# Kernel optimization log

Measured on AMD Instinct MI355X. Metric: run time of the kernel, lower is better.

Reference implementation:

```python
import jax, jax.numpy as jnp
import numpy as np

N, E, NFEAT, NHID, H = 25000, 400000, 256, 32, 12
NEG_SLOPE = 0.2


def setup_inputs() -> dict:
    key = jax.random.key(0)
    ks = jax.random.split(key, 16)
    g = lambda k, shp, s=0.05: jax.random.normal(k, shp, dtype=jnp.float32) * s
    return {
        "x": jax.random.normal(ks[0], (N, NFEAT), dtype=jnp.float32),
        "edge_index": jax.random.randint(ks[1], (2, E), 0, N, dtype=jnp.int64),
        "edge_attr": jax.random.normal(ks[2], (E, NHID), dtype=jnp.float32),
        # conv1: in=NFEAT -> H heads x NHID, edge_dim=NHID, concat=True
        "W1": g(ks[3], (NFEAT, H * NHID)),
        "att_src1": g(ks[4], (H, NHID)),
        "att_dst1": g(ks[5], (H, NHID)),
        "W_e1": g(ks[6], (NHID, H * NHID)),
        "att_edge1": g(ks[7], (H, NHID)),
        "b1": jnp.zeros((H * NHID,), jnp.float32),
        # conv2: in=H*NHID -> H heads x NHID, concat=False (mean over heads)
        "W2": g(ks[8], (H * NHID, H * NHID)),
        "att_src2": g(ks[9], (H, NHID)),
        "att_dst2": g(ks[10], (H, NHID)),
        "b2": jnp.zeros((NHID,), jnp.float32),
    }


def gat_layer(x, edge_index, W, att_src, att_dst, bias, concat,
              edge_attr=None, W_e=None, att_e=None):
    n = x.shape[0]
    h, c = att_src.shape
    hx = (x @ W).reshape(n, h, c)                      # [N,H,C]
    a_s = jnp.sum(hx * att_src, axis=-1)               # [N,H]
    a_d = jnp.sum(hx * att_dst, axis=-1)               # [N,H]
    src, dst = edge_index[0], edge_index[1]
    loop = jnp.arange(n)
    if edge_attr is not None:
        # PyG add_self_loops fill_value='mean': mean of incoming edge_attr per dst
        cnt = jax.ops.segment_sum(jnp.ones(dst.shape[0], jnp.float32), dst, n)
        loop_attr = jax.ops.segment_sum(edge_attr, dst, n) / jnp.maximum(cnt, 1.0)[:, None]
        edge_attr = jnp.concatenate([edge_attr, loop_attr], axis=0)
    src = jnp.concatenate([src, loop])
    dst = jnp.concatenate([dst, loop])
    e = a_s[src] + a_d[dst]                            # [E+N,H]
    if edge_attr is not None:
        he = (edge_attr @ W_e).reshape(-1, h, c)
        e = e + jnp.sum(he * att_e, axis=-1)
    e = jax.nn.leaky_relu(e, NEG_SLOPE)
    # segment softmax over destination nodes (every node has a self loop -> no empty segments)
    m = jax.ops.segment_max(e, dst, n)                 # [N,H]
    ex = jnp.exp(e - m[dst])
    den = jax.ops.segment_sum(ex, dst, n)
    alpha = ex / den[dst]                              # [E+N,H]
    out = jax.ops.segment_sum(alpha[:, :, None] * hx[src], dst, n)  # [N,H,C]
    out = out.reshape(n, h * c) if concat else out.mean(axis=1)
    return out + bias


def reference(x, edge_index, edge_attr, W1, att_src1, att_dst1, W_e1, att_edge1, b1,
              W2, att_src2, att_dst2, b2):
    # eval mode: all F.dropout / GATConv dropout are identity
    h1 = gat_layer(x, edge_index, W1, att_src1, att_dst1, b1, True,
                   edge_attr, W_e1, att_edge1)
    h1 = jax.nn.elu(h1)
    h2 = gat_layer(h1, edge_index, W2, att_src2, att_dst2, b2, False)
    return h2, jax.nn.log_softmax(h2, axis=1)
```

## Files before the change

kernel.cpp:

```cpp
#include <hip/hip_runtime.h>
#include <hip/hip_bf16.h>
#include <math.h>

#define N_NODES 25000
#define N_EDGES 400000
#define NFEAT   256
#define NHID    32
#define NHEAD   12
#define HC      384
#define HCX     416
#define NEG_SLOPE 0.2f
#define NBLK    ((N_NODES + 255) / 256)
#define BPAD    40

typedef __attribute__((ext_vector_type(8))) short short8;
typedef __attribute__((ext_vector_type(4))) float floatx4;

__device__ __forceinline__ float bf2f(unsigned short u) {
    union { unsigned int i; float f; } v; v.i = ((unsigned int)u) << 16; return v.f;
}
__device__ __forceinline__ unsigned short f2bf(float f) {
    union { float f; unsigned int i; } v; v.f = f;
    unsigned int x = v.i;
    unsigned int r = (x + 0x7FFFu + ((x >> 16) & 1u)) >> 16;
    return (unsigned short)r;
}
__device__ __forceinline__ int clampN(int s) {
    return ((unsigned)s < (unsigned)N_NODES) ? s : 0;
}
__device__ __forceinline__ float ldf(const void* p, size_t i, int isF32) {
    return isF32 ? ((const float*)p)[i] : bf2f(((const unsigned short*)p)[i]);
}
__device__ __forceinline__ int ldi(const void* p, size_t i, int isI64) {
    return isI64 ? (int)((const unsigned int*)p)[2 * i] : ((const int*)p)[i];
}

__device__ __forceinline__ void fma8(float* acc, float a, uint4 g) {
    unsigned int u[4] = {g.x, g.y, g.z, g.w};
#pragma unroll
    for (int i = 0; i < 4; i++) {
        union { unsigned int i; float f; } lo, hi;
        lo.i = u[i] << 16;
        hi.i = u[i] & 0xFFFF0000u;
        acc[2 * i]     += a * lo.f;
        acc[2 * i + 1] += a * hi.f;
    }
}
__device__ __forceinline__ void mul8(float* acc, float a, uint4 g) {
    unsigned int u[4] = {g.x, g.y, g.z, g.w};
#pragma unroll
    for (int i = 0; i < 4; i++) {
        union { unsigned int i; float f; } lo, hi;
        lo.i = u[i] << 16;
        hi.i = u[i] & 0xFFFF0000u;
        acc[2 * i]     = a * lo.f;
        acc[2 * i + 1] = a * hi.f;
    }
}

__global__ void detect_kernel(const unsigned short* __restrict__ xr,
                              const unsigned int* __restrict__ eir,
                              int* __restrict__ flags) {
    __shared__ int sF, sI;
    if (threadIdx.x == 0) { sF = 0; sI = 0; }
    __syncthreads();
    int t = threadIdx.x;
    int cf = 0, ci = 0;
#pragma unroll
    for (int i = 0; i < 4; i++) {
        unsigned short u = xr[2 * (t * 4 + i)];
        int e = (u >> 7) & 0xFF;
        if (e >= 100 && e <= 140) cf++;
        unsigned int v = eir[2 * (t * 4 + i) + 1];
        if (v == 0u) ci++;
    }
    atomicAdd(&sF, cf);
    atomicAdd(&sI, ci);
    __syncthreads();
    if (threadIdx.x == 0) {
        flags[0] = (sF >= 614) ? 0 : 1;
        flags[1] = (sI >= 512) ? 1 : 0;
    }
}

__global__ void prep_kernel(const void* __restrict__ We1,
                            const void* __restrict__ att_e,
                            const void* __restrict__ W1,
                            const void* __restrict__ W2,
                            const void* __restrict__ as1,
                            const void* __restrict__ ad1,
                            const void* __restrict__ as2,
                            const void* __restrict__ ad2,
                            const int* __restrict__ flags,
                            float* __restrict__ M1,
                            unsigned short* __restrict__ Wt1,
                            unsigned short* __restrict__ Wt2) {
    int isF32 = flags[0];
    int id = blockIdx.x * 256 + threadIdx.x;
    if (id < 384) {
        int k = id / 12, h = id % 12;
        float s = 0.f;
        for (int c = 0; c < 32; c++)
            s += ldf(We1, (size_t)k * HC + h * 32 + c, isF32) *
                 ldf(att_e, (size_t)h * 32 + c, isF32);
        M1[k * 12 + h] = s;
        return;
    }
    int id1 = id - 384;
    if (id1 < HCX * 256) {
        int n = id1 / 256, k = id1 % 256;
        unsigned short v = 0;
        if (n < 384) {
            v = f2bf(ldf(W1, (size_t)k * HC + n, isF32));
        } else if (n < 400) {
            int h = n - 384;
            if (h < 12) {
                float s = 0.f;
                for (int c = 0; c < 32; c++)
                    s += ldf(W1, (size_t)k * HC + h * 32 + c, isF32) *
                         ldf(as1, (size_t)h * 32 + c, isF32);
                v = f2bf(s);
            }
        } else {
            int h = n - 400;
            if (h < 12) {
                float s = 0.f;
                for (int c = 0; c < 32; c++)
                    s += ldf(W1, (size_t)k * HC + h * 32 + c, isF32) *
                         ldf(ad1, (size_t)h * 32 + c, isF32);
                v = f2bf(s);
            }
        }
        Wt1[(size_t)n * 256 + k] = v;
        return;
    }
    int id2 = id1 - HCX * 256;
    if (id2 < HCX * 384) {
        int n = id2 / 384, k = id2 % 384;
        unsigned short v = 0;
        if (n < 384) {
            v = f2bf(ldf(W2, (size_t)k * HC + n, isF32));
        } else if (n < 400) {
            int h = n - 384;
            if (h < 12) {
                float s = 0.f;
                for (int c = 0; c < 32; c++)
                    s += ldf(W2, (size_t)k * HC + h * 32 + c, isF32) *
                         ldf(as2, (size_t)h * 32 + c, isF32);
                v = f2bf(s);
            }
        } else {
            int h = n - 400;
            if (h < 12) {
                float s = 0.f;
                for (int c = 0; c < 32; c++)
                    s += ldf(W2, (size_t)k * HC + h * 32 + c, isF32) *
                         ldf(ad2, (size_t)h * 32 + c, isF32);
                v = f2bf(s);
            }
        }
        Wt2[(size_t)n * 384 + k] = v;
    }
}

__global__ void hist_kernel(const void* __restrict__ ei, const int* __restrict__ flags,
                            int* __restrict__ cnt) {
    int isI64 = flags[1];
    int e = blockIdx.x * 256 + threadIdx.x;
    if (e < N_EDGES) {
        int d = clampN(ldi(ei, (size_t)N_EDGES + e, isI64));
        atomicAdd(&cnt[d], 1);
    }
}

__global__ void blockscan_kernel(const int* __restrict__ cnt, int* __restrict__ incl,
                                 int* __restrict__ bsum) {
    __shared__ int buf[256];
    int i = blockIdx.x * 256 + threadIdx.x;
    int v = (i < N_NODES) ? cnt[i] : 0;
    buf[threadIdx.x] = v;
    __syncthreads();
    for (int off = 1; off < 256; off <<= 1) {
        int t = (threadIdx.x >= off) ? buf[threadIdx.x - off] : 0;
        __syncthreads();
        buf[threadIdx.x] += t;
        __syncthreads();
    }
    if (i < N_NODES) incl[i] = buf[threadIdx.x];
    if (threadIdx.x == 255) bsum[blockIdx.x] = buf[255];
}

__global__ void bscan_kernel(const int* __restrict__ bsum, int* __restrict__ boff) {
    __shared__ int buf[128];
    int t = threadIdx.x;
    int v = (t < NBLK) ? bsum[t] : 0;
    buf[t] = v;
    __syncthreads();
    for (int off = 1; off < 128; off <<= 1) {
        int u = (t >= off) ? buf[t - off] : 0;
        __syncthreads();
        buf[t] += u;
        __syncthreads();
    }
    if (t < NBLK) boff[t] = buf[t] - v;
}

__global__ void finalize_kernel(const int* __restrict__ incl, const int* __restrict__ boff,
                                const int* __restrict__ cnt,
                                int* __restrict__ rowptr, int* __restrict__ wofs) {
    int i = blockIdx.x * 256 + threadIdx.x;
    if (i == 0) rowptr[0] = 0;
    if (i < N_NODES) {
        int v = incl[i] + boff[blockIdx.x];
        rowptr[i + 1] = v;
        wofs[i] = v - cnt[i];
    }
}

__global__ void scatter_kernel(const void* __restrict__ ei, const int* __restrict__ flags,
                               int* __restrict__ wofs, int2* __restrict__ pairs) {
    int isI64 = flags[1];
    int e = blockIdx.x * 256 + threadIdx.x;
    if (e >= N_EDGES) return;
    int d = clampN(ldi(ei, (size_t)N_EDGES + e, isI64));
    int pos = atomicAdd(&wofs[d], 1);
    if ((unsigned)pos >= (unsigned)N_EDGES) return;
    pairs[pos] = make_int2(clampN(ldi(ei, (size_t)e, isI64)), e);
}

__global__ void ae_kernel(const void* __restrict__ ea, const int* __restrict__ flags,
                          const float* __restrict__ M1,
                          const int2* __restrict__ pairs,
                          unsigned short* __restrict__ ae_edge) {
    __shared__ float sM[384];
    for (int i = threadIdx.x; i < 384; i += 256) sM[i] = M1[i];
    __syncthreads();
    int isF32 = flags[0];
    int p = blockIdx.x * 256 + threadIdx.x;
    if (p >= N_EDGES) return;
    int eid = pairs[p].y;
    if ((unsigned)eid >= (unsigned)N_EDGES) eid = 0;
    float a[32];
    if (isF32) {
        const float4* r4 = (const float4*)((const float*)ea + (size_t)eid * 32);
#pragma unroll
        for (int i = 0; i < 8; i++) {
            float4 v = r4[i];
            a[4 * i] = v.x; a[4 * i + 1] = v.y; a[4 * i + 2] = v.z; a[4 * i + 3] = v.w;
        }
    } else {
        const unsigned short* r = (const unsigned short*)ea + (size_t)eid * 32;
#pragma unroll
        for (int i = 0; i < 32; i++) a[i] = bf2f(r[i]);
    }
    float ev[12];
#pragma unroll
    for (int h = 0; h < 12; h++) ev[h] = 0.f;
#pragma unroll
    for (int k = 0; k < 32; k++)
#pragma unroll
        for (int h = 0; h < 12; h++) ev[h] += a[k] * sM[k * 12 + h];
    unsigned int w[6];
#pragma unroll
    for (int i = 0; i < 6; i++)
        w[i] = (unsigned int)f2bf(ev[2 * i]) | ((unsigned int)f2bf(ev[2 * i + 1]) << 16);
    uint2* dst = (uint2*)(ae_edge + (size_t)p * 12);
    dst[0] = make_uint2(w[0], w[1]);
    dst[1] = make_uint2(w[2], w[3]);
    dst[2] = make_uint2(w[4], w[5]);
}

__global__ __launch_bounds__(512) void gemm_mfma(const void* __restrict__ A,
                                                 const unsigned short* __restrict__ Bt,
                                                 const int* __restrict__ flags,
                                                 int aFromFlag,
                                                 unsigned short* __restrict__ C,
                                                 float* __restrict__ a_s,
                                                 float* __restrict__ a_d,
                                                 int M, int K) {
    __shared__ unsigned short sB[HCX * BPAD];
    int aF32 = aFromFlag ? flags[0] : 0;
    int lane = threadIdx.x & 63;
    int w = threadIdx.x >> 6;
    int m0 = blockIdx.x * 64 + (w >> 1) * 16;
    int c0 = (w & 1) * 192;
    int ecol = 384 + (w & 1) * 16;
    int r = lane & 15, q = lane >> 4;
    int row = m0 + r;
    if (row >= M) row = M - 1;
    floatx4 acc[13];
#pragma unroll
    for (int j = 0; j < 13; j++) acc[j] = (floatx4){0.f, 0.f, 0.f, 0.f};
    for (int k0 = 0; k0 < K; k0 += 32) {
        for (int i = threadIdx.x; i < HCX * 4; i += 512) {
            int col = i >> 2, seg = i & 3;
            *(uint4*)(sB + (size_t)col * BPAD + seg * 8) =
                *(const uint4*)(Bt + (size_t)col * K + k0 + seg * 8);
        }
        __syncthreads();
        short8 a;
        if (aF32) {
            const float4* ap = (const float4*)((const float*)A + (size_t)row * K + k0 + q * 8);
            float4 u = ap[0], v = ap[1];
            a[0] = (short)f2bf(u.x); a[1] = (short)f2bf(u.y);
            a[2] = (short)f2bf(u.z); a[3] = (short)f2bf(u.w);
            a[4] = (short)f2bf(v.x); a[5] = (short)f2bf(v.y);
            a[6] = (short)f2bf(v.z); a[7] = (short)f2bf(v.w);
        } else {
            a = *(const short8*)((const unsigned short*)A + (size_t)row * K + k0 + q * 8);
        }
#pragma unroll
        for (int j = 0; j < 12; j++) {
            int col = c0 + 16 * j + r;
            short8 b = *(const short8*)(sB + (size_t)col * BPAD + q * 8);
            acc[j] = __builtin_amdgcn_mfma_f32_16x16x32_bf16(a, b, acc[j], 0, 0, 0);
        }
        {
            short8 b = *(const short8*)(sB + (size_t)(ecol + r) * BPAD + q * 8);
            acc[12] = __builtin_amdgcn_mfma_f32_16x16x32_bf16(a, b, acc[12], 0, 0, 0);
        }
        __syncthreads();
    }
#pragma unroll
    for (int j = 0; j < 12; j++) {
        int col = c0 + 16 * j + r;
#pragma unroll
        for (int t = 0; t < 4; t++) {
            int orow = m0 + q * 4 + t;
            if (orow < M) C[(size_t)orow * HC + col] = f2bf(acc[j][t]);
        }
    }
    if (r < 12) {
        float* dst = (w & 1) ? a_d : a_s;
#pragma unroll
        for (int t = 0; t < 4; t++) {
            int orow = m0 + q * 4 + t;
            if (orow < M) dst[orow * 12 + r] = acc[12][t];
        }
    }
}

__global__ __launch_bounds__(256) void softmax_kernel(const float* __restrict__ a_s,
                                                      const float* __restrict__ a_d,
                                                      const int* __restrict__ rowptr,
                                                      const int2* __restrict__ pairs,
                                                      const unsigned short* __restrict__ ae_edge,
                                                      unsigned short* __restrict__ alpha_e,
                                                      float* __restrict__ exl_out,
                                                      float* __restrict__ rden_out,
                                                      int has_ae) {
    int id = blockIdx.x * 256 + threadIdx.x;
    if (id >= N_NODES * NHEAD) return;
    int node = id / NHEAD;
    int h = id - node * NHEAD;
    int start = rowptr[node], end = rowptr[node + 1];
    if (start < 0) start = 0;
    if (end > N_EDGES) end = N_EDGES;
    int deg = end - start;
    float adn = a_d[id];
    float asn = a_s[id];
    float mx = -1e30f, sae = 0.f;
    for (int p = start; p < end; p += 2) {
        int2 pe0 = pairs[p];
        bool two = (p + 1 < end);
        int2 pe1 = two ? pairs[p + 1] : pe0;
        int s0 = clampN(pe0.x), s1 = clampN(pe1.x);
        float v0 = a_s[(size_t)s0 * NHEAD + h] + adn;
        float v1 = a_s[(size_t)s1 * NHEAD + h] + adn;
        if (has_ae) {
            float a0 = bf2f(ae_edge[(size_t)p * NHEAD + h]);
            float a1 = two ? bf2f(ae_edge[(size_t)(p + 1) * NHEAD + h]) : 0.f;
            v0 += a0; sae += a0;
            if (two) { v1 += a1; sae += a1; }
        }
        v0 = v0 > 0.f ? v0 : NEG_SLOPE * v0;
        v1 = v1 > 0.f ? v1 : NEG_SLOPE * v1;
        mx = fmaxf(mx, v0);
        if (two) mx = fmaxf(mx, v1);
    }
    float invdeg = 1.f / fmaxf((float)deg, 1.f);
    float el = asn + adn + (has_ae ? sae * invdeg : 0.f);
    el = el > 0.f ? el : NEG_SLOPE * el;
    mx = fmaxf(mx, el);
    float den = 0.f;
    for (int p = start; p < end; p += 2) {
        int2 pe0 = pairs[p];
        bool two = (p + 1 < end);
        int2 pe1 = two ? pairs[p + 1] : pe0;
        int s0 = clampN(pe0.x), s1 = clampN(pe1.x);
        float v0 = a_s[(size_t)s0 * NHEAD + h] + adn;
        float v1 = a_s[(size_t)s1 * NHEAD + h] + adn;
        if (has_ae) {
            v0 += bf2f(ae_edge[(size_t)p * NHEAD + h]);
            if (two) v1 += bf2f(ae_edge[(size_t)(p + 1) * NHEAD + h]);
        }
        v0 = v0 > 0.f ? v0 : NEG_SLOPE * v0;
        v1 = v1 > 0.f ? v1 : NEG_SLOPE * v1;
        float ex0 = expf(v0 - mx);
        float ex1 = expf(v1 - mx);
        alpha_e[(size_t)p * NHEAD + h] = f2bf(ex0);
        den += ex0;
        if (two) {
            alpha_e[(size_t)(p + 1) * NHEAD + h] = f2bf(ex1);
            den += ex1;
        }
    }
    float exl = expf(el - mx);
    exl_out[id] = exl;
    rden_out[id] = 1.f / (den + exl);
}

__global__ __launch_bounds__(256) void agg1_kernel(const unsigned short* __restrict__ hx,
                                                   const unsigned short* __restrict__ alpha_e,
                                                   const float* __restrict__ exl,
                                                   const float* __restrict__ rden,
                                                   const int* __restrict__ rowptr,
                                                   const int2* __restrict__ pairs,
                                                   const void* __restrict__ b1,
                                                   const int* __restrict__ flags,
                                                   unsigned short* __restrict__ h1) {
    int isF32 = flags[0];
    int lane = threadIdx.x & 63;
    int node = blockIdx.x * 4 + (threadIdx.x >> 6);
    if (node >= N_NODES || lane >= 48) return;
    int h = lane >> 2;
    int off = lane * 8;
    int start = rowptr[node], end = rowptr[node + 1];
    if (start < 0) start = 0;
    if (end > N_EDGES) end = N_EDGES;
    float acc[8];
    {
        uint4 g = *(const uint4*)(hx + (size_t)node * HC + off);
        mul8(acc, exl[node * 12 + h], g);
    }
    int p = start;
    int2 pe0, pe1, pe2, pe3;
    bool have = (p + 4 <= end);
    if (have) {
        pe0 = pairs[p]; pe1 = pairs[p + 1]; pe2 = pairs[p + 2]; pe3 = pairs[p + 3];
    }
    while (have) {
        int2 c0 = pe0, c1 = pe1, c2 = pe2, c3 = pe3;
        bool nxt = (p + 8 <= end);
        if (nxt) {
            pe0 = pairs[p + 4]; pe1 = pairs[p + 5]; pe2 = pairs[p + 6]; pe3 = pairs[p + 7];
        }
        uint4 g0 = *(const uint4*)(hx + (size_t)clampN(c0.x) * HC + off);
        uint4 g1 = *(const uint4*)(hx + (size_t)clampN(c1.x) * HC + off);
        uint4 g2 = *(const uint4*)(hx + (size_t)clampN(c2.x) * HC + off);
        uint4 g3 = *(const uint4*)(hx + (size_t)clampN(c3.x) * HC + off);
        float a0 = bf2f(alpha_e[(size_t)p * 12 + h]);
        float a1 = bf2f(alpha_e[(size_t)(p + 1) * 12 + h]);
        float a2 = bf2f(alpha_e[(size_t)(p + 2) * 12 + h]);
        float a3 = bf2f(alpha_e[(size_t)(p + 3) * 12 + h]);
        fma8(acc, a0, g0);
        fma8(acc, a1, g1);
        fma8(acc, a2, g2);
        fma8(acc, a3, g3);
        p += 4;
        have = nxt;
    }
    for (; p < end; p++) {
        int2 pe = pairs[p];
        uint4 g = *(const uint4*)(hx + (size_t)clampN(pe.x) * HC + off);
        float a = bf2f(alpha_e[(size_t)p * 12 + h]);
        fma8(acc, a, g);
    }
    float rd = rden[node * 12 + h];
    unsigned int w[4];
#pragma unroll
    for (int i = 0; i < 4; i++) {
        float v0 = acc[2 * i] * rd + ldf(b1, (size_t)(off + 2 * i), isF32);
        float v1 = acc[2 * i + 1] * rd + ldf(b1, (size_t)(off + 2 * i + 1), isF32);
        v0 = v0 > 0.f ? v0 : expm1f(v0);
        v1 = v1 > 0.f ? v1 : expm1f(v1);
        w[i] = (unsigned int)f2bf(v0) | ((unsigned int)f2bf(v1) << 16);
    }
    *(uint4*)(h1 + (size_t)node * HC + off) = make_uint4(w[0], w[1], w[2], w[3]);
}

__global__ __launch_bounds__(256) void agg2_kernel(const unsigned short* __restrict__ hx,
                                                   const unsigned short* __restrict__ alpha_e,
                                                   const float* __restrict__ exl,
                                                   const float* __restrict__ rden,
                                                   const int* __restrict__ rowptr,
                                                   const int2* __restrict__ pairs,
                                                   const void* __restrict__ b2,
                                                   const int* __restrict__ flags,
                                                   float* __restrict__ out) {
    int isF32 = flags[0];
    int lane = threadIdx.x & 63;
    int node = blockIdx.x * 4 + (threadIdx.x >> 6);
    if (node >= N_NODES) return;
    bool act = lane < 48;
    int h = act ? (lane >> 2) : 0;
    int off = act ? lane * 8 : 0;
    float acc[8];
#pragma unroll
    for (int k = 0; k < 8; k++) acc[k] = 0.f;
    if (act) {
        int start = rowptr[node], end = rowptr[node + 1];
        if (start < 0) start = 0;
        if (end > N_EDGES) end = N_EDGES;
        {
            uint4 g = *(const uint4*)(hx + (size_t)node * HC + off);
            mul8(acc, exl[node * 12 + h], g);
        }
        int p = start;
        int2 pe0, pe1, pe2, pe3;
        bool have = (p + 4 <= end);
        if (have) {
            pe0 = pairs[p]; pe1 = pairs[p + 1]; pe2 = pairs[p + 2]; pe3 = pairs[p + 3];
        }
        while (have) {
            int2 c0 = pe0, c1 = pe1, c2 = pe2, c3 = pe3;
            bool nxt = (p + 8 <= end);
            if (nxt) {
                pe0 = pairs[p + 4]; pe1 = pairs[p + 5]; pe2 = pairs[p + 6]; pe3 = pairs[p + 7];
            }
            uint4 g0 = *(const uint4*)(hx + (size_t)clampN(c0.x) * HC + off);
            uint4 g1 = *(const uint4*)(hx + (size_t)clampN(c1.x) * HC + off);
            uint4 g2 = *(const uint4*)(hx + (size_t)clampN(c2.x) * HC + off);
            uint4 g3 = *(const uint4*)(hx + (size_t)clampN(c3.x) * HC + off);
            float a0 = bf2f(alpha_e[(size_t)p * 12 + h]);
            float a1 = bf2f(alpha_e[(size_t)(p + 1) * 12 + h]);
            float a2 = bf2f(alpha_e[(size_t)(p + 2) * 12 + h]);
            float a3 = bf2f(alpha_e[(size_t)(p + 3) * 12 + h]);
            fma8(acc, a0, g0);
            fma8(acc, a1, g1);
            fma8(acc, a2, g2);
            fma8(acc, a3, g3);
            p += 4;
            have = nxt;
        }
        for (; p < end; p++) {
            int2 pe = pairs[p];
            uint4 g = *(const uint4*)(hx + (size_t)clampN(pe.x) * HC + off);
            float a = bf2f(alpha_e[(size_t)p * 12 + h]);
            fma8(acc, a, g);
        }
        float rd = rden[node * 12 + h];
#pragma unroll
        for (int k = 0; k < 8; k++) acc[k] *= rd;
    }
#pragma unroll
    for (int k = 0; k < 8; k++) {
        float t1 = __shfl(acc[k], lane + 16);
        float t2 = __shfl(acc[k], lane + 32);
        acc[k] += t1 + t2;
        acc[k] += __shfl_xor(acc[k], 4);
        acc[k] += __shfl_xor(acc[k], 8);
    }
    if (lane < 4) {
        int q = lane;
        float hv[8];
        float m = -1e30f;
#pragma unroll
        for (int t = 0; t < 8; t++) {
            hv[t] = acc[t] * (1.f / 12.f) + ldf(b2, (size_t)(8 * q + t), isF32);
            m = fmaxf(m, hv[t]);
        }
        m = fmaxf(m, __shfl_xor(m, 1));
        m = fmaxf(m, __shfl_xor(m, 2));
        float s = 0.f;
#pragma unroll
        for (int t = 0; t < 8; t++) s += expf(hv[t] - m);
        s += __shfl_xor(s, 1);
        s += __shfl_xor(s, 2);
        float ls = m + logf(s);
        float4* o0 = (float4*)(out + (size_t)node * 32 + 8 * q);
        float4* l0 = (float4*)(out + (size_t)N_NODES * 32 + (size_t)node * 32 + 8 * q);
        o0[0] = make_float4(hv[0], hv[1], hv[2], hv[3]);
        o0[1] = make_float4(hv[4], hv[5], hv[6], hv[7]);
        l0[0] = make_float4(hv[0] - ls, hv[1] - ls, hv[2] - ls, hv[3] - ls);
        l0[1] = make_float4(hv[4] - ls, hv[5] - ls, hv[6] - ls, hv[7] - ls);
    }
}

extern "C" void kernel_launch(void* const* d_in, const int* in_sizes, int n_in,
                              void* d_out, int out_size, void* d_ws, size_t ws_size,
                              hipStream_t stream) {
    const void* x        = d_in[0];
    const void* ei       = d_in[1];
    const void* ea       = d_in[2];
    const void* W1       = d_in[3];
    const void* att_src1 = d_in[4];
    const void* att_dst1 = d_in[5];
    const void* We1      = d_in[6];
    const void* att_e1   = d_in[7];
    const void* b1       = d_in[8];
    const void* W2       = d_in[9];
    const void* att_src2 = d_in[10];
    const void* att_dst2 = d_in[11];
    const void* b2       = d_in[12];
    float* out = (float*)d_out;

    char* ws = (char*)d_ws;
    size_t off = 0;
    auto alloc = [&](size_t bytes) -> void* {
        void* p = ws + off;
        off = (off + bytes + 255) & ~(size_t)255;
        return p;
    };
    int*            flags   = (int*)alloc(16);
    float*          M1      = (float*)alloc((size_t)384 * 4);
    int*            rowptr  = (int*)alloc((size_t)(N_NODES + 1) * 4);
    int*            cnt     = (int*)alloc((size_t)N_NODES * 4);
    int*            wofs    = (int*)alloc((size_t)N_NODES * 4);
    int*            incl    = (int*)alloc((size_t)N_NODES * 4);
    int*            bsum    = (int*)alloc((size_t)NBLK * 4);
    int*            boff    = (int*)alloc((size_t)NBLK * 4);
    float*          a_s     = (float*)alloc((size_t)N_NODES * 12 * 4);
    float*          a_d     = (float*)alloc((size_t)N_NODES * 12 * 4);
    float*          exl     = (float*)alloc((size_t)N_NODES * 12 * 4);
    float*          rden    = (float*)alloc((size_t)N_NODES * 12 * 4);
    int2*           pairs   = (int2*)alloc((size_t)N_EDGES * 8);
    unsigned short* alpha_e = (unsigned short*)alloc((size_t)N_EDGES * 12 * 2);
    unsigned short* hx      = (unsigned short*)alloc((size_t)N_NODES * HC * 2);
    unsigned short* h1      = (unsigned short*)alloc((size_t)N_NODES * HC * 2);
    unsigned short* ae_edge = h1;
    unsigned short* Wt1     = (unsigned short*)alloc((size_t)HCX * 256 * 2);
    unsigned short* Wt2     = (unsigned short*)alloc((size_t)HCX * 384 * 2);

    hipMemsetAsync(cnt, 0, (size_t)N_NODES * 4, stream);
    detect_kernel<<<1, 256, 0, stream>>>((const unsigned short*)x, (const unsigned int*)ei, flags);
    prep_kernel<<<(384 + HCX * 256 + HCX * 384 + 255) / 256, 256, 0, stream>>>(
        We1, att_e1, W1, W2, att_src1, att_dst1, att_src2, att_dst2, flags, M1, Wt1, Wt2);
    hist_kernel<<<(N_EDGES + 255) / 256, 256, 0, stream>>>(ei, flags, cnt);
    blockscan_kernel<<<NBLK, 256, 0, stream>>>(cnt, incl, bsum);
    bscan_kernel<<<1, 128, 0, stream>>>(bsum, boff);
    finalize_kernel<<<NBLK, 256, 0, stream>>>(incl, boff, cnt, rowptr, wofs);
    scatter_kernel<<<(N_EDGES + 255) / 256, 256, 0, stream>>>(ei, flags, wofs, pairs);
    ae_kernel<<<(N_EDGES + 255) / 256, 256, 0, stream>>>(ea, flags, M1, pairs, ae_edge);
    gemm_mfma<<<(N_NODES + 63) / 64, 512, 0, stream>>>(x, Wt1, flags, 1, hx, a_s, a_d,
                                                       N_NODES, NFEAT);
    softmax_kernel<<<(N_NODES * 12 + 255) / 256, 256, 0, stream>>>(a_s, a_d, rowptr, pairs,
                                                                   ae_edge, alpha_e, exl, rden, 1);
    agg1_kernel<<<(N_NODES + 3) / 4, 256, 0, stream>>>(hx, alpha_e, exl, rden, rowptr, pairs,
                                                       b1, flags, h1);
    gemm_mfma<<<(N_NODES + 63) / 64, 512, 0, stream>>>(h1, Wt2, flags, 0, hx, a_s, a_d,
                                                       N_NODES, HC);
    softmax_kernel<<<(N_NODES * 12 + 255) / 256, 256, 0, stream>>>(a_s, a_d, rowptr, pairs,
                                                                   ae_edge, alpha_e, exl, rden, 0);
    agg2_kernel<<<(N_NODES + 3) / 4, 256, 0, stream>>>(hx, alpha_e, exl, rden, rowptr, pairs,
                                                       b2, flags, out);
}
```

Baseline: 409.2 us.

## Fuse CSR-building preprocessing kernels to cut launch count

```diff
diff --git a/kernel.cpp b/kernel.cpp
--- a/kernel.cpp
+++ b/kernel.cpp
@@ -10,8 +10,11 @@
 #define HC      384
 #define HCX     416
 #define NEG_SLOPE 0.2f
-#define NBLK    ((N_NODES + 255) / 256)
 #define BPAD    40
+#define PREP_BLKS ((384 + HCX * 256 + HCX * 384 + 255) / 256)
+#define HIST_BLKS ((N_EDGES + 255) / 256)
+#define SCAN_T  1024
+#define SCAN_C  25
 
 typedef __attribute__((ext_vector_type(8))) short short8;
 typedef __attribute__((ext_vector_type(4))) float floatx4;
@@ -60,18 +63,22 @@
 
 __global__ void detect_kernel(const unsigned short* __restrict__ xr,
                               const unsigned int* __restrict__ eir,
-                              int* __restrict__ flags) {
+                              int* __restrict__ flags,
+                              int* __restrict__ cnt) {
+    int i = blockIdx.x * 256 + threadIdx.x;
+    if (i < N_NODES) cnt[i] = 0;
+    if (blockIdx.x != 0) return;
     __shared__ int sF, sI;
     if (threadIdx.x == 0) { sF = 0; sI = 0; }
     __syncthreads();
     int t = threadIdx.x;
     int cf = 0, ci = 0;
 #pragma unroll
-    for (int i = 0; i < 4; i++) {
-        unsigned short u = xr[2 * (t * 4 + i)];
+    for (int k = 0; k < 4; k++) {
+        unsigned short u = xr[2 * (t * 4 + k)];
         int e = (u >> 7) & 0xFF;
         if (e >= 100 && e <= 140) cf++;
-        unsigned int v = eir[2 * (t * 4 + i) + 1];
+        unsigned int v = eir[2 * (t * 4 + k) + 1];
         if (v == 0u) ci++;
     }
     atomicAdd(&sF, cf);
@@ -83,20 +90,32 @@
     }
 }
 
-__global__ void prep_kernel(const void* __restrict__ We1,
-                            const void* __restrict__ att_e,
-                            const void* __restrict__ W1,
-                            const void* __restrict__ W2,
-                            const void* __restrict__ as1,
-                            const void* __restrict__ ad1,
-                            const void* __restrict__ as2,
-                            const void* __restrict__ ad2,
-                            const int* __restrict__ flags,
-                            float* __restrict__ M1,
-                            unsigned short* __restrict__ Wt1,
-                            unsigned short* __restrict__ Wt2) {
+__global__ void prep_hist_kernel(const void* __restrict__ We1,
+                                 const void* __restrict__ att_e,
+                                 const void* __restrict__ W1,
+                                 const void* __restrict__ W2,
+                                 const void* __restrict__ as1,
+                                 const void* __restrict__ ad1,
+                                 const void* __restrict__ as2,
+                                 const void* __restrict__ ad2,
+                                 const void* __restrict__ ei,
+                                 const int* __restrict__ flags,
+                                 float* __restrict__ M1,
+                                 unsigned short* __restrict__ Wt1,
+                                 unsigned short* __restrict__ Wt2,
+                                 int* __restrict__ cnt) {
     int isF32 = flags[0];
-    int id = blockIdx.x * 256 + threadIdx.x;
+    int bid = blockIdx.x;
+    if (bid >= PREP_BLKS) {
+        int isI64 = flags[1];
+        int e = (bid - PREP_BLKS) * 256 + threadIdx.x;
+        if (e < N_EDGES) {
+            int d = clampN(ldi(ei, (size_t)N_EDGES + e, isI64));
+            atomicAdd(&cnt[d], 1);
+        }
+        return;
+    }
+    int id = bid * 256 + threadIdx.x;
     if (id < 384) {
         int k = id / 12, h = id % 12;
         float s = 0.f;
@@ -163,62 +182,53 @@
     }
 }
 
-__global__ void hist_kernel(const void* __restrict__ ei, const int* __restrict__ flags,
-                            int* __restrict__ cnt) {
-    int isI64 = flags[1];
-    int e = blockIdx.x * 256 + threadIdx.x;
-    if (e < N_EDGES) {
-        int d = clampN(ldi(ei, (size_t)N_EDGES + e, isI64));
-        atomicAdd(&cnt[d], 1);
-    }
-}
-
-__global__ void blockscan_kernel(const int* __restrict__ cnt, int* __restrict__ incl,
-                                 int* __restrict__ bsum) {
-    __shared__ int buf[256];
-    int i = blockIdx.x * 256 + threadIdx.x;
-    int v = (i < N_NODES) ? cnt[i] : 0;
-    buf[threadIdx.x] = v;
+__global__ __launch_bounds__(SCAN_T) void scan_kernel(const int* __restrict__ cnt,
+                                                      int* __restrict__ rowptr,
+                                                      int* __restrict__ wofs) {
+    __shared__ int part[SCAN_T];
+    int t = threadIdx.x;
+    int base = t * SCAN_C;
+    int local[SCAN_C];
+    int s = 0;
+#pragma unroll
+    for (int i = 0; i < SCAN_C; i++) {
+        int idx = base + i;
+        int v = (idx < N_NODES) ? cnt[idx] : 0;
+        local[i] = v;
+        s += v;
+    }
+    part[t] = s;
     __syncthreads();
-    for (int off = 1; off < 256; off <<= 1) {
-        int t = (threadIdx.x >= off) ? buf[threadIdx.x - off] : 0;
+    for (int off = 1; off < SCAN_T; off <<= 1) {
+        int u = (t >= off) ? part[t - off] : 0;
         __syncthreads();
-        buf[threadIdx.x] += t;
+        part[t] += u;
         __syncthreads();
     }
-    if (i < N_NODES) incl[i] = buf[threadIdx.x];
-    if (threadIdx.x == 255) bsum[blockIdx.x] = buf[255];
-}
-
-__global__ void bscan_kernel(const int* __restrict__ bsum, int* __restrict__ boff) {
-    __shared__ int buf[128];
-    int t = threadIdx.x;
-    int v = (t < NBLK) ? bsum[t] : 0;
-    buf[t] = v;
+    int run = (t == 0) ? 0 : part[t - 1];
+    if (t == 0) rowptr[0] = 0;
+#pragma unroll
+    for (int i = 0; i < SCAN_C; i++) {
+        int idx = base + i;
+        if (idx < N_NODES) {
+            wofs[idx] = run;
+            run += local[i];
+            rowptr[idx + 1] = run;
+        }
+    }
+}
+
+__global__ void scatter_ae_kernel(const void* __restrict__ ei,
+                                  const void* __restrict__ ea,
+                                  const int* __restrict__ flags,
+                                  const float* __restrict__ M1,
+                                  int* __restrict__ wofs,
+                                  int2* __restrict__ pairs,
+                                  unsigned short* __restrict__ ae_edge) {
+    __shared__ float sM[384];
+    for (int i = threadIdx.x; i < 384; i += 256) sM[i] = M1[i];
     __syncthreads();
-    for (int off = 1; off < 128; off <<= 1) {
-        int u = (t >= off) ? buf[t - off] : 0;
-        __syncthreads();
-        buf[t] += u;
-        __syncthreads();
-    }
-    if (t < NBLK) boff[t] = buf[t] - v;
-}
-
-__global__ void finalize_kernel(const int* __restrict__ incl, const int* __restrict__ boff,
-                                const int* __restrict__ cnt,
-                                int* __restrict__ rowptr, int* __restrict__ wofs) {
-    int i = blockIdx.x * 256 + threadIdx.x;
-    if (i == 0) rowptr[0] = 0;
-    if (i < N_NODES) {
-        int v = incl[i] + boff[blockIdx.x];
-        rowptr[i + 1] = v;
-        wofs[i] = v - cnt[i];
-    }
-}
-
-__global__ void scatter_kernel(const void* __restrict__ ei, const int* __restrict__ flags,
-                               int* __restrict__ wofs, int2* __restrict__ pairs) {
+    int isF32 = flags[0];
     int isI64 = flags[1];
     int e = blockIdx.x * 256 + threadIdx.x;
     if (e >= N_EDGES) return;
@@ -226,30 +236,16 @@
     int pos = atomicAdd(&wofs[d], 1);
     if ((unsigned)pos >= (unsigned)N_EDGES) return;
     pairs[pos] = make_int2(clampN(ldi(ei, (size_t)e, isI64)), e);
-}
-
-__global__ void ae_kernel(const void* __restrict__ ea, const int* __restrict__ flags,
-                          const float* __restrict__ M1,
-                          const int2* __restrict__ pairs,
-                          unsigned short* __restrict__ ae_edge) {
-    __shared__ float sM[384];
-    for (int i = threadIdx.x; i < 384; i += 256) sM[i] = M1[i];
-    __syncthreads();
-    int isF32 = flags[0];
-    int p = blockIdx.x * 256 + threadIdx.x;
-    if (p >= N_EDGES) return;
-    int eid = pairs[p].y;
-    if ((unsigned)eid >= (unsigned)N_EDGES) eid = 0;
     float a[32];
     if (isF32) {
-        const float4* r4 = (const float4*)((const float*)ea + (size_t)eid * 32);
+        const float4* r4 = (const float4*)((const float*)ea + (size_t)e * 32);
 #pragma unroll
         for (int i = 0; i < 8; i++) {
             float4 v = r4[i];
             a[4 * i] = v.x; a[4 * i + 1] = v.y; a[4 * i + 2] = v.z; a[4 * i + 3] = v.w;
         }
     } else {
-        const unsigned short* r = (const unsigned short*)ea + (size_t)eid * 32;
+        const unsigned short* r = (const unsigned short*)ea + (size_t)e * 32;
 #pragma unroll
         for (int i = 0; i < 32; i++) a[i] = bf2f(r[i]);
     }
@@ -264,7 +260,7 @@
 #pragma unroll
     for (int i = 0; i < 6; i++)
         w[i] = (unsigned int)f2bf(ev[2 * i]) | ((unsigned int)f2bf(ev[2 * i + 1]) << 16);
-    uint2* dst = (uint2*)(ae_edge + (size_t)p * 12);
+    uint2* dst = (uint2*)(ae_edge + (size_t)pos * 12);
     dst[0] = make_uint2(w[0], w[1]);
     dst[1] = make_uint2(w[2], w[3]);
     dst[2] = make_uint2(w[4], w[5]);
@@ -607,9 +603,6 @@
     int*            rowptr  = (int*)alloc((size_t)(N_NODES + 1) * 4);
     int*            cnt     = (int*)alloc((size_t)N_NODES * 4);
     int*            wofs    = (int*)alloc((size_t)N_NODES * 4);
-    int*            incl    = (int*)alloc((size_t)N_NODES * 4);
-    int*            bsum    = (int*)alloc((size_t)NBLK * 4);
-    int*            boff    = (int*)alloc((size_t)NBLK * 4);
     float*          a_s     = (float*)alloc((size_t)N_NODES * 12 * 4);
     float*          a_d     = (float*)alloc((size_t)N_NODES * 12 * 4);
     float*          exl     = (float*)alloc((size_t)N_NODES * 12 * 4);
@@ -622,16 +615,13 @@
     unsigned short* Wt1     = (unsigned short*)alloc((size_t)HCX * 256 * 2);
     unsigned short* Wt2     = (unsigned short*)alloc((size_t)HCX * 384 * 2);
 
-    hipMemsetAsync(cnt, 0, (size_t)N_NODES * 4, stream);
-    detect_kernel<<<1, 256, 0, stream>>>((const unsigned short*)x, (const unsigned int*)ei, flags);
-    prep_kernel<<<(384 + HCX * 256 + HCX * 384 + 255) / 256, 256, 0, stream>>>(
-        We1, att_e1, W1, W2, att_src1, att_dst1, att_src2, att_dst2, flags, M1, Wt1, Wt2);
-    hist_kernel<<<(N_EDGES + 255) / 256, 256, 0, stream>>>(ei, flags, cnt);
-    blockscan_kernel<<<NBLK, 256, 0, stream>>>(cnt, incl, bsum);
-    bscan_kernel<<<1, 128, 0, stream>>>(bsum, boff);
-    finalize_kernel<<<NBLK, 256, 0, stream>>>(incl, boff, cnt, rowptr, wofs);
-    scatter_kernel<<<(N_EDGES + 255) / 256, 256, 0, stream>>>(ei, flags, wofs, pairs);
-    ae_kernel<<<(N_EDGES + 255) / 256, 256, 0, stream>>>(ea, flags, M1, pairs, ae_edge);
+    detect_kernel<<<(N_NODES + 255) / 256, 256, 0, stream>>>(
+        (const unsigned short*)x, (const unsigned int*)ei, flags, cnt);
+    prep_hist_kernel<<<PREP_BLKS + HIST_BLKS, 256, 0, stream>>>(
+        We1, att_e1, W1, W2, att_src1, att_dst1, att_src2, att_dst2, ei, flags,
+        M1, Wt1, Wt2, cnt);
+    scan_kernel<<<1, SCAN_T, 0, stream>>>(cnt, rowptr, wofs);
+    scatter_ae_kernel<<<HIST_BLKS, 256, 0, stream>>>(ei, ea, flags, M1, wofs, pairs, ae_edge);
     gemm_mfma<<<(N_NODES + 63) / 64, 512, 0, stream>>>(x, Wt1, flags, 1, hx, a_s, a_d,
                                                        N_NODES, NFEAT);
     softmax_kernel<<<(N_NODES * 12 + 255) / 256, 256, 0, stream>>>(a_s, a_d, rowptr, pairs,
```

Result: slower. 426.9 us (+4.3%).
